# Performance work log

Measured on AMD Instinct MI355X. Metric: run time of the kernel, lower is better.

## Reference

```python
import jax, jax.numpy as jnp
import numpy as np

B, S, D, MD = 4, 4096, 1024, 512
SCALE = 0.02  # init scale for weights


def _layernorm(x, g, b, eps=1e-5):
    m = jnp.mean(x, axis=-1, keepdims=True)
    v = jnp.mean((x - m) ** 2, axis=-1, keepdims=True)
    return (x - m) * jax.lax.rsqrt(v + eps) * g + b


def _mem_mlp(h, W0, W1):
    # MemoryMLP depth=2: linear -> gelu -> linear (no biases)
    return jax.nn.gelu(h @ W0) @ W1


def _assoc_scan(gates, inputs):
    # state_t = g_t * state_{t-1} + in_t, over the seq axis (axis=1)
    def step(state, gi):
        g, i = gi
        s = g * state + i
        return s, s
    init = jnp.zeros_like(inputs[:, 0])
    _, out = jax.lax.scan(step, init, (jnp.moveaxis(gates, 1, 0), jnp.moveaxis(inputs, 1, 0)))
    return jnp.moveaxis(out, 1, 0)


def setup_inputs() -> dict:
    key = jax.random.key(0)
    ks = jax.random.split(key, 10)
    return {
        "x": jax.random.normal(ks[0], (B, S, D), jnp.float32),
        "Wd": jax.random.normal(ks[1], (D, MD), jnp.float32) * SCALE,
        "bd": jnp.zeros((MD,), jnp.float32),
        "Wu": jax.random.normal(ks[2], (MD, D), jnp.float32) * SCALE,
        "bu": jnp.zeros((D,), jnp.float32),
        "Wq": jax.random.normal(ks[3], (MD, MD), jnp.float32) * SCALE,
        "bq": jnp.zeros((MD,), jnp.float32),
        "Wk": jax.random.normal(ks[4], (MD, MD), jnp.float32) * SCALE,
        "bk": jnp.zeros((MD,), jnp.float32),
        "Wv": jax.random.normal(ks[5], (MD, MD), jnp.float32) * SCALE,
        "bv": jnp.zeros((MD,), jnp.float32),
        "q_gamma": jnp.ones((MD,), jnp.float32),
        "q_beta": jnp.zeros((MD,), jnp.float32),
        "k_gamma": jnp.ones((MD,), jnp.float32),
        "k_beta": jnp.zeros((MD,), jnp.float32),
        "W0": jax.random.normal(ks[6], (MD, MD), jnp.float32) * SCALE,
        "W1": jax.random.normal(ks[7], (MD, MD), jnp.float32) * SCALE,
        "adaptive_lr": jnp.full((1,), 0.01, jnp.float32),
        "forget_factor": jnp.full((1,), 0.1, jnp.float32),
    }


def reference(x, Wd, bd, Wu, bu, Wq, bq, Wk, bk, Wv, bv,
              q_gamma, q_beta, k_gamma, k_beta, W0, W1,
              adaptive_lr, forget_factor):
    h = x @ Wd + bd                                   # [B,S,MD] down_proj
    q = _layernorm(h @ Wq + bq, q_gamma, q_beta)      # q_norm(to_queries)
    k = _layernorm(h @ Wk + bk, k_gamma, k_beta)      # k_norm(to_keys)
    v = h @ Wv + bv                                   # to_values
    retrieved = _mem_mlp(q, W0, W1)                   # memory read
    pred = _mem_mlp(k, W0, W1)                        # memory store pred
    # per-token surprise: MSE over feature dim
    surprise = jnp.mean((pred - v) ** 2, axis=-1, keepdims=True)  # [B,S,1]
    gate_val = 1.0 - jax.nn.sigmoid(forget_factor)[0]
    gates = jnp.full((B, S, 1), 1.0, jnp.float32) * gate_val
    inputs = adaptive_lr[0] * surprise * v            # surprise-weighted write
    scanned = _assoc_scan(gates, inputs)              # sequential recurrence
    out = (retrieved + scanned) @ Wu + bu             # up_proj
    return out
```

## Files before the change

kernel.cpp:

```cpp
#include <hip/hip_runtime.h>
#include <hip/hip_bf16.h>
#include <math.h>

#define B_    4
#define S_    4096
#define DD    1024
#define MD    512
#define NTOK  16384
#define CHUNK 32
#define NCH   128

typedef unsigned short u16;
typedef unsigned int u32;
typedef __attribute__((ext_vector_type(8))) short short8;
typedef __attribute__((ext_vector_type(4))) float f32x4;
typedef __attribute__((ext_vector_type(4))) unsigned short us4;

__device__ __forceinline__ float bf2f(u16 u) {
    u32 x = ((u32)u) << 16;
    return __builtin_bit_cast(float, x);
}
__device__ __forceinline__ u16 f2bf(float f) {
    u32 x = __builtin_bit_cast(u32, f);
    u32 lsb = (x >> 16) & 1u;
    x += 0x7fffu + lsb;
    return (u16)(x >> 16);
}
__device__ __forceinline__ float gelu_f(float x) {
    float x3 = x * x * x;
    return 0.5f * x * (1.0f + tanhf(0.7978845608028654f * (x + 0.044715f * x3)));
}
__device__ __forceinline__ float gate_from_ff(const float* ff) {
    return 1.0f - 1.0f / (1.0f + expf(-ff[0]));
}

#define GLDS(gp, lp) __builtin_amdgcn_global_load_lds( \
    (const __attribute__((address_space(1))) void*)(gp), \
    (__attribute__((address_space(3))) void*)(lp), 16, 0, 0)

__device__ __forceinline__ int swzoff(int row, int byteInRow) {
    return ((row * 128 + byteInRow) ^ ((row & 7) << 4)) >> 1;
}

template<int EPI, int HB, int OUTBF>
__global__ __launch_bounds__(256) void gemm_bf16_k(
    const u16* __restrict__ A, const u16* __restrict__ BT,
    const float* __restrict__ bias, void* __restrict__ outp,
    int K, int gx, int OM)
{
    __shared__ __align__(16) u16 Al[2][128 * 64];
    __shared__ __align__(16) u16 Bl[2][128 * 64];
    const int tid = threadIdx.x;
    const int w = tid >> 6, l = tid & 63;

    const int nwg = gridDim.x;
    const int cpx = nwg >> 3;
    const int o = blockIdx.x;
    const int swz = (o & 7) * cpx + (o >> 3);
    const int bx = swz % gx, by = swz / gx;

    const int rowBase = by * 128, colBase = bx * 128;
    const int wm = (w >> 1) * 64, wn = (w & 1) * 64;

    const int srow = l >> 3;
    const int skoff = ((l & 7) ^ (l >> 3)) * 8;
    const u16* Ag[4];
    const u16* Bg[4];
#pragma unroll
    for (int j = 0; j < 4; ++j) {
        const int seg = w * 4 + j;
        Ag[j] = A  + (size_t)(rowBase + seg * 8 + srow) * K + skoff;
        Bg[j] = BT + (size_t)(colBase + seg * 8 + srow) * K + skoff;
    }

    f32x4 acc[4][4];
#pragma unroll
    for (int i = 0; i < 4; ++i)
#pragma unroll
        for (int j = 0; j < 4; ++j) acc[i][j] = (f32x4){0.f, 0.f, 0.f, 0.f};

    const int KT = K >> 6;

#define STAGE(kt, buf) do { \
    const size_t ko = (size_t)(kt) << 6; \
    _Pragma("unroll") \
    for (int j = 0; j < 4; ++j) { \
        GLDS(Ag[j] + ko, &Al[buf][(w * 4 + j) * 512]); \
        GLDS(Bg[j] + ko, &Bl[buf][(w * 4 + j) * 512]); \
    } \
} while (0)

    STAGE(0, 0);
    __syncthreads();

    const int lr = l & 15;
    const int gb = (l >> 4) * 16;
    int cur = 0;
    for (int kt = 0; kt < KT; ++kt) {
        if (kt + 1 < KT) STAGE(kt + 1, cur ^ 1);
#pragma unroll
        for (int ks = 0; ks < 2; ++ks) {
            short8 af[4], bfr[4];
#pragma unroll
            for (int m = 0; m < 4; ++m)
                af[m] = *(const short8*)&Al[cur][swzoff(wm + m * 16 + lr, ks * 64 + gb)];
#pragma unroll
            for (int n = 0; n < 4; ++n)
                bfr[n] = *(const short8*)&Bl[cur][swzoff(wn + n * 16 + lr, ks * 64 + gb)];
#pragma unroll
            for (int m = 0; m < 4; ++m)
#pragma unroll
                for (int n = 0; n < 4; ++n)
                    acc[m][n] = __builtin_amdgcn_mfma_f32_16x16x32_bf16(af[m], bfr[n], acc[m][n], 0, 0, 0);
        }
        __syncthreads();
        cur ^= 1;
    }
#undef STAGE

    const int g4 = (l >> 4) * 4;
    const int col0 = colBase + wn;

    if (OUTBF) {
        u16* scr = &Al[0][0] + w * 1024;
        u16* ob = (u16*)outp;
        const bool odd = l & 1;
        const int lrp = lr & ~1;
#pragma unroll
        for (int m = 0; m < 4; ++m) {
            const int baseRow = rowBase + wm + m * 16;
            float vq[4][4];
#pragma unroll
            for (int n = 0; n < 4; ++n) {
                const float bj = HB ? bias[col0 + n * 16 + lr] : 0.0f;
#pragma unroll
                for (int q = 0; q < 4; ++q) {
                    float vv = acc[m][n][q] + bj;
                    if (EPI == 1) vv = gelu_f(vv);
                    vq[n][q] = vv;
                }
            }
#pragma unroll
            for (int n = 0; n < 4; ++n) {
                float pv[4];
#pragma unroll
                for (int q = 0; q < 4; ++q) pv[q] = __shfl_xor(vq[n][q], 1);
                const int q0 = odd ? 2 : 0;
#pragma unroll
                for (int j = 0; j < 2; ++j) {
                    const int qq = q0 + j;
                    float lo = odd ? pv[qq] : vq[n][qq];
                    float hi = odd ? vq[n][qq] : pv[qq];
                    u32 word = (u32)f2bf(lo) | ((u32)f2bf(hi) << 16);
                    *(u32*)&scr[(g4 + qq) * 64 + n * 16 + lrp] = word;
                }
            }
            asm volatile("s_waitcnt lgkmcnt(0)" ::: "memory");
            __builtin_amdgcn_sched_barrier(0);
            short8 r0 = *(const short8*)&scr[(l >> 3) * 64 + (l & 7) * 8];
            short8 r1 = *(const short8*)&scr[((l >> 3) + 8) * 64 + (l & 7) * 8];
            const size_t gaddr = (size_t)(baseRow + (l >> 3)) * OM + col0 + (l & 7) * 8;
            *(short8*)(ob + gaddr) = r0;
            *(short8*)(ob + gaddr + (size_t)8 * OM) = r1;
            __builtin_amdgcn_sched_barrier(0);
        }
    } else {
#pragma unroll
        for (int n = 0; n < 4; ++n) {
            const int col = col0 + n * 16 + lr;
            const float bj = HB ? bias[col] : 0.0f;
#pragma unroll
            for (int m = 0; m < 4; ++m) {
                const int row0 = rowBase + wm + m * 16 + g4;
#pragma unroll
                for (int q = 0; q < 4; ++q) {
                    float vv = acc[m][n][q] + bj;
                    if (EPI == 1) vv = gelu_f(vv);
                    ((float*)outp)[(size_t)(row0 + q) * OM + col] = vv;
                }
            }
        }
    }
}

__global__ __launch_bounds__(256) void cvt_bf16_k(const float* __restrict__ in,
                                                  u16* __restrict__ out, int n)
{
    size_t i = ((size_t)blockIdx.x * 256 + threadIdx.x) * 8;
    if (i + 8 > (size_t)n) return;
    float4 a = *(const float4*)(in + i);
    float4 b = *(const float4*)(in + i + 4);
    short8 o;
    o[0] = (short)f2bf(a.x); o[1] = (short)f2bf(a.y);
    o[2] = (short)f2bf(a.z); o[3] = (short)f2bf(a.w);
    o[4] = (short)f2bf(b.x); o[5] = (short)f2bf(b.y);
    o[6] = (short)f2bf(b.z); o[7] = (short)f2bf(b.w);
    *(short8*)(out + i) = o;
}

__global__ __launch_bounds__(256) void wtrans_k(const float* __restrict__ W,
                                                u16* __restrict__ WT, int K, int M)
{
    __shared__ float t[32][33];
    const int tx = threadIdx.x, ty = threadIdx.y;
    const int m0 = blockIdx.x * 32, k0 = blockIdx.y * 32;
#pragma unroll
    for (int i = 0; i < 4; ++i)
        t[ty + i * 8][tx] = W[(size_t)(k0 + ty + i * 8) * M + m0 + tx];
    __syncthreads();
#pragma unroll
    for (int i = 0; i < 4; ++i)
        WT[(size_t)(m0 + ty + i * 8) * K + k0 + tx] = f2bf(t[tx][ty + i * 8]);
}

__global__ __launch_bounds__(256) void wtrans5_k(
    const float* __restrict__ Wa, const float* __restrict__ Wb,
    const float* __restrict__ Wc, const float* __restrict__ Wd_,
    const float* __restrict__ We,
    u16* __restrict__ Ta, u16* __restrict__ Tb, u16* __restrict__ Tc,
    u16* __restrict__ Td, u16* __restrict__ Te)
{
    __shared__ float t[32][33];
    const float* W; u16* T;
    switch (blockIdx.z) {
        case 0: W = Wa; T = Ta; break;
        case 1: W = Wb; T = Tb; break;
        case 2: W = Wc; T = Tc; break;
        case 3: W = Wd_; T = Td; break;
        default: W = We; T = Te; break;
    }
    const int tx = threadIdx.x, ty = threadIdx.y;
    const int m0 = blockIdx.x * 32, k0 = blockIdx.y * 32;
#pragma unroll
    for (int i = 0; i < 4; ++i)
        t[ty + i * 8][tx] = W[(size_t)(k0 + ty + i * 8) * 512 + m0 + tx];
    __syncthreads();
#pragma unroll
    for (int i = 0; i < 4; ++i)
        T[(size_t)(m0 + ty + i * 8) * 512 + k0 + tx] = f2bf(t[tx][ty + i * 8]);
}

__global__ __launch_bounds__(256) void ln2_k(u16* __restrict__ X0, u16* __restrict__ X1,
                                             const float* __restrict__ g0, const float* __restrict__ b0,
                                             const float* __restrict__ g1, const float* __restrict__ b1)
{
    const int row = blockIdx.x, tid = threadIdx.x;
    u16* x = (blockIdx.y ? X1 : X0) + (size_t)row * MD;
    const float* g = blockIdx.y ? g1 : g0;
    const float* b = blockIdx.y ? b1 : b0;
    float v0 = bf2f(x[tid]), v1 = bf2f(x[tid + 256]);
    float s = v0 + v1, q = v0 * v0 + v1 * v1;
#pragma unroll
    for (int off = 32; off > 0; off >>= 1) {
        s += __shfl_down(s, off);
        q += __shfl_down(q, off);
    }
    __shared__ float redS[4], redQ[4];
    __shared__ float s_mean, s_rstd;
    const int lane = tid & 63, w = tid >> 6;
    if (lane == 0) { redS[w] = s; redQ[w] = q; }
    __syncthreads();
    if (tid == 0) {
        float S = redS[0] + redS[1] + redS[2] + redS[3];
        float Q = redQ[0] + redQ[1] + redQ[2] + redQ[3];
        float m = S * (1.f / 512.f);
        float var = Q * (1.f / 512.f) - m * m;
        s_mean = m; s_rstd = rsqrtf(var + 1e-5f);
    }
    __syncthreads();
    const float m = s_mean, rs = s_rstd;
    x[tid]       = f2bf((v0 - m) * rs * g[tid]       + b[tid]);
    x[tid + 256] = f2bf((v1 - m) * rs * g[tid + 256] + b[tid + 256]);
}

__global__ __launch_bounds__(256) void surprise_k(const u16* __restrict__ pred,
                                                  const u16* __restrict__ v,
                                                  const float* __restrict__ lr_p,
                                                  float* __restrict__ coef)
{
    const int row = blockIdx.x, tid = threadIdx.x;
    const u16* pp = pred + (size_t)row * MD;
    const u16* vp = v + (size_t)row * MD;
    float d0 = bf2f(pp[tid]) - bf2f(vp[tid]);
    float d1 = bf2f(pp[tid + 256]) - bf2f(vp[tid + 256]);
    float q = d0 * d0 + d1 * d1;
#pragma unroll
    for (int off = 32; off > 0; off >>= 1) q += __shfl_down(q, off);
    __shared__ float redQ[4];
    const int lane = tid & 63, w = tid >> 6;
    if (lane == 0) redQ[w] = q;
    __syncthreads();
    if (tid == 0) {
        float Q = redQ[0] + redQ[1] + redQ[2] + redQ[3];
        coef[row] = lr_p[0] * (Q * (1.f / 512.f));
    }
}

__global__ __launch_bounds__(256) void scan1_k(u16* __restrict__ io,
                                               const float* __restrict__ coef,
                                               const float* __restrict__ ff,
                                               float* __restrict__ carry)
{
    const int idx = blockIdx.x * blockDim.x + threadIdx.x;
    const int d4 = (idx & 127) * 4;
    const int c = (idx >> 7) & (NCH - 1);
    const int b = idx >> 14;
    const float g = gate_from_ff(ff);
    const int tok0 = b * S_ + c * CHUNK;
    u16* p = io + (size_t)tok0 * MD + d4;
    const float* cf = coef + tok0;
    float s0 = 0.f, s1 = 0.f, s2 = 0.f, s3 = 0.f;
#pragma unroll 4
    for (int t = 0; t < CHUNK; ++t) {
        us4 vv = *(const us4*)(p + (size_t)t * MD);
        const float ct = cf[t];
        s0 = fmaf(g, s0, ct * bf2f(vv.x));
        s1 = fmaf(g, s1, ct * bf2f(vv.y));
        s2 = fmaf(g, s2, ct * bf2f(vv.z));
        s3 = fmaf(g, s3, ct * bf2f(vv.w));
        us4 ov = { f2bf(s0), f2bf(s1), f2bf(s2), f2bf(s3) };
        *(us4*)(p + (size_t)t * MD) = ov;
    }
    float4 cw = { s0, s1, s2, s3 };
    *(float4*)(carry + ((size_t)b * NCH + c) * MD + d4) = cw;
}

__global__ __launch_bounds__(256) void scan2_k(const float* __restrict__ carry,
                                               const float* __restrict__ ff,
                                               float* __restrict__ Sin)
{
    const int idx = blockIdx.x * blockDim.x + threadIdx.x;
    const int d = idx & (MD - 1);
    const int b = idx >> 9;
    const float g = gate_from_ff(ff);
    const float gL = powf(g, (float)CHUNK);
    float p = 0.f;
    for (int c = 0; c < NCH; ++c) {
        Sin[((size_t)b * NCH + c) * MD + d] = p;
        p = carry[((size_t)b * NCH + c) * MD + d] + gL * p;
    }
}

__global__ __launch_bounds__(256) void scan3_k(const u16* __restrict__ loc,
                                               const float* __restrict__ Sin,
                                               const u16* __restrict__ retr,
                                               const float* __restrict__ ff,
                                               u16* __restrict__ fin)
{
    const size_t idx = (size_t)blockIdx.x * blockDim.x + threadIdx.x;
    const int d4 = (int)(idx & 127) * 4;
    const int t = (int)((idx >> 7) & (S_ - 1));
    const int b = (int)(idx >> 19);
    const int c = t >> 5, tl = t & (CHUNK - 1);
    const float g = gate_from_ff(ff);
    const float f = exp2f((float)(tl + 1) * log2f(g));
    const size_t row = (size_t)(b * S_ + t) * MD + d4;
    us4 lv = *(const us4*)(loc + row);
    us4 rv = *(const us4*)(retr + row);
    float4 sv = *(const float4*)(Sin + ((size_t)b * NCH + c) * MD + d4);
    us4 ov;
    ov.x = f2bf(bf2f(lv.x) + f * sv.x + bf2f(rv.x));
    ov.y = f2bf(bf2f(lv.y) + f * sv.y + bf2f(rv.y));
    ov.z = f2bf(bf2f(lv.z) + f * sv.z + bf2f(rv.z));
    ov.w = f2bf(bf2f(lv.w) + f * sv.w + bf2f(rv.w));
    *(us4*)(fin + row) = ov;
}

extern "C" void kernel_launch(void* const* d_in, const int* in_sizes, int n_in,
                              void* d_out, int out_size, void* d_ws, size_t ws_size,
                              hipStream_t stream) {
    const float* x   = (const float*)d_in[0];
    const float* Wd  = (const float*)d_in[1];
    const float* bd  = (const float*)d_in[2];
    const float* Wu  = (const float*)d_in[3];
    const float* bu  = (const float*)d_in[4];
    const float* Wq  = (const float*)d_in[5];
    const float* bq  = (const float*)d_in[6];
    const float* Wk  = (const float*)d_in[7];
    const float* bk  = (const float*)d_in[8];
    const float* Wv  = (const float*)d_in[9];
    const float* bv  = (const float*)d_in[10];
    const float* qg  = (const float*)d_in[11];
    const float* qb  = (const float*)d_in[12];
    const float* kg  = (const float*)d_in[13];
    const float* kb  = (const float*)d_in[14];
    const float* W0  = (const float*)d_in[15];
    const float* W1  = (const float*)d_in[16];
    const float* lr  = (const float*)d_in[17];
    const float* ff  = (const float*)d_in[18];
    float* out = (float*)d_out;

    u16* wdT   = (u16*)d_ws;
    u16* wqT   = wdT + 512 * 1024;
    u16* wkT   = wqT + 512 * 512;
    u16* wvT   = wkT + 512 * 512;
    u16* w0T   = wvT + 512 * 512;
    u16* w1T   = w0T + 512 * 512;
    u16* wuT   = w1T + 512 * 512;
    u16* xb    = wuT + 1024 * 512;
    u16* hb    = xb + (size_t)NTOK * DD;
    u16* b1    = hb + (size_t)NTOK * MD;
    u16* b2    = b1 + (size_t)NTOK * MD;
    u16* VB    = b2 + (size_t)NTOK * MD;
    u16* ax    = VB + (size_t)NTOK * MD;
    float* coef  = (float*)(ax + (size_t)NTOK * MD);
    float* carry = coef + NTOK;
    float* Sin   = carry + (size_t)B_ * NCH * MD;

    dim3 blk(256);
    dim3 t32(32, 8);

    cvt_bf16_k<<<(NTOK * DD) / (256 * 8), blk, 0, stream>>>(x, xb, NTOK * DD);
    wtrans_k<<<dim3(16, 32), t32, 0, stream>>>(Wd, wdT, 1024, 512);
    wtrans5_k<<<dim3(16, 16, 5), t32, 0, stream>>>(Wq, Wk, Wv, W0, W1,
        wqT, wkT, wvT, w0T, w1T);
    wtrans_k<<<dim3(32, 16), t32, 0, stream>>>(Wu, wuT, 512, 1024);

    gemm_bf16_k<0, 1, 1><<<dim3(512), blk, 0, stream>>>(xb, wdT, bd, hb, 1024, 4, 512);
    gemm_bf16_k<0, 1, 1><<<dim3(512), blk, 0, stream>>>(hb, wqT, bq, b1, 512, 4, 512);
    gemm_bf16_k<0, 1, 1><<<dim3(512), blk, 0, stream>>>(hb, wkT, bk, b2, 512, 4, 512);
    gemm_bf16_k<0, 1, 1><<<dim3(512), blk, 0, stream>>>(hb, wvT, bv, VB, 512, 4, 512);
    ln2_k<<<dim3(NTOK, 2), blk, 0, stream>>>(b1, b2, qg, qb, kg, kb);
    gemm_bf16_k<1, 0, 1><<<dim3(512), blk, 0, stream>>>(b1, w0T, nullptr, ax, 512, 4, 512);
    gemm_bf16_k<0, 0, 1><<<dim3(512), blk, 0, stream>>>(ax, w1T, nullptr, b1, 512, 4, 512);
    gemm_bf16_k<1, 0, 1><<<dim3(512), blk, 0, stream>>>(b2, w0T, nullptr, ax, 512, 4, 512);
    gemm_bf16_k<0, 0, 1><<<dim3(512), blk, 0, stream>>>(ax, w1T, nullptr, b2, 512, 4, 512);
    surprise_k<<<NTOK, blk, 0, stream>>>(b2, VB, lr, coef);
    scan1_k<<<(B_ * NCH * (MD / 4)) / 256, blk, 0, stream>>>(VB, coef, ff, carry);
    scan2_k<<<(B_ * MD) / 256, blk, 0, stream>>>(carry, ff, Sin);
    scan3_k<<<(NTOK * (MD / 4)) / 256, blk, 0, stream>>>(VB, Sin, b1, ff, ax);
    gemm_bf16_k<0, 1, 0><<<dim3(1024), blk, 0, stream>>>(ax, wuT, bu, out, 512, 8, 1024);
}
```

Measured before the change: 332.8 us.

## Batch independent GEMMs via grid z and use 3-stage BK=32 pipeline

The GEMM kernel now takes three operand sets selected by blockIdx.z, so the Q/K/V projections run as one launch and the two memory-MLP passes are paired per layer. The mainloop switches from a double-buffered K-tile of 64 to a triple-buffered K-tile of 32, with explicit vmcnt waits and a single barrier per step so loads for two tiles ahead overlap compute. Bias is loaded before the loop, and the scratch buffers are reused from xb and hb to make room for two MLP intermediates. This cuts launch count and tail effects and raises occupancy through smaller LDS use, at the cost of more barriers per unit of K work.

```diff
diff --git a/kernel.cpp b/kernel.cpp
--- a/kernel.cpp
+++ b/kernel.cpp
@@ -38,20 +38,24 @@
     (const __attribute__((address_space(1))) void*)(gp), \
     (__attribute__((address_space(3))) void*)(lp), 16, 0, 0)
 
-__device__ __forceinline__ int swzoff(int row, int byteInRow) {
-    return ((row * 128 + byteInRow) ^ ((row & 7) << 4)) >> 1;
-}
-
 template<int EPI, int HB, int OUTBF>
 __global__ __launch_bounds__(256) void gemm_bf16_k(
-    const u16* __restrict__ A, const u16* __restrict__ BT,
-    const float* __restrict__ bias, void* __restrict__ outp,
+    const u16* __restrict__ A0, const u16* __restrict__ A1, const u16* __restrict__ A2,
+    const u16* __restrict__ W0p, const u16* __restrict__ W1p, const u16* __restrict__ W2p,
+    const float* __restrict__ c0, const float* __restrict__ c1, const float* __restrict__ c2,
+    void* __restrict__ o0, void* __restrict__ o1, void* __restrict__ o2,
     int K, int gx, int OM)
 {
-    __shared__ __align__(16) u16 Al[2][128 * 64];
-    __shared__ __align__(16) u16 Bl[2][128 * 64];
+    __shared__ __align__(16) u16 Al[3][128 * 32];
+    __shared__ __align__(16) u16 Bl[3][128 * 32];
     const int tid = threadIdx.x;
     const int w = tid >> 6, l = tid & 63;
+
+    const int z = blockIdx.z;
+    const u16* A      = (z == 0) ? A0 : (z == 1) ? A1 : A2;
+    const u16* BT     = (z == 0) ? W0p : (z == 1) ? W1p : W2p;
+    const float* bias = (z == 0) ? c0 : (z == 1) ? c1 : c2;
+    void* outp        = (z == 0) ? o0 : (z == 1) ? o1 : o2;
 
     const int nwg = gridDim.x;
     const int cpx = nwg >> 3;
@@ -61,17 +65,23 @@
 
     const int rowBase = by * 128, colBase = bx * 128;
     const int wm = (w >> 1) * 64, wn = (w & 1) * 64;
-
-    const int srow = l >> 3;
-    const int skoff = ((l & 7) ^ (l >> 3)) * 8;
-    const u16* Ag[4];
-    const u16* Bg[4];
-#pragma unroll
-    for (int j = 0; j < 4; ++j) {
-        const int seg = w * 4 + j;
-        Ag[j] = A  + (size_t)(rowBase + seg * 8 + srow) * K + skoff;
-        Bg[j] = BT + (size_t)(colBase + seg * 8 + srow) * K + skoff;
-    }
+    const int lr = l & 15;
+
+    float bj[4] = {0.f, 0.f, 0.f, 0.f};
+    if (HB) {
+#pragma unroll
+        for (int n = 0; n < 4; ++n) bj[n] = bias[colBase + wn + n * 16 + lr];
+        asm volatile("" :: "v"(bj[0]), "v"(bj[1]), "v"(bj[2]), "v"(bj[3]));
+    }
+    asm volatile("s_waitcnt vmcnt(0)" ::: "memory");
+    __builtin_amdgcn_sched_barrier(0);
+
+    const int srow = l >> 2;
+    const int skoff = ((l & 3) ^ (srow & 3)) * 8;
+    const u16* Ag0 = A  + (size_t)(rowBase + w * 16 + srow) * K + skoff;
+    const u16* Ag1 = A  + (size_t)(rowBase + (w + 4) * 16 + srow) * K + skoff;
+    const u16* Bg0 = BT + (size_t)(colBase + w * 16 + srow) * K + skoff;
+    const u16* Bg1 = BT + (size_t)(colBase + (w + 4) * 16 + srow) * K + skoff;
 
     f32x4 acc[4][4];
 #pragma unroll
@@ -79,42 +89,47 @@
 #pragma unroll
         for (int j = 0; j < 4; ++j) acc[i][j] = (f32x4){0.f, 0.f, 0.f, 0.f};
 
-    const int KT = K >> 6;
+    const int KT = K >> 5;
 
 #define STAGE(kt, buf) do { \
-    const size_t ko = (size_t)(kt) << 6; \
-    _Pragma("unroll") \
-    for (int j = 0; j < 4; ++j) { \
-        GLDS(Ag[j] + ko, &Al[buf][(w * 4 + j) * 512]); \
-        GLDS(Bg[j] + ko, &Bl[buf][(w * 4 + j) * 512]); \
-    } \
+    const size_t ko = (size_t)(kt) << 5; \
+    GLDS(Ag0 + ko, &Al[buf][(w * 16) * 32]); \
+    GLDS(Ag1 + ko, &Al[buf][((w + 4) * 16) * 32]); \
+    GLDS(Bg0 + ko, &Bl[buf][(w * 16) * 32]); \
+    GLDS(Bg1 + ko, &Bl[buf][((w + 4) * 16) * 32]); \
 } while (0)
 
     STAGE(0, 0);
-    __syncthreads();
-
-    const int lr = l & 15;
-    const int gb = (l >> 4) * 16;
-    int cur = 0;
-    for (int kt = 0; kt < KT; ++kt) {
-        if (kt + 1 < KT) STAGE(kt + 1, cur ^ 1);
-#pragma unroll
-        for (int ks = 0; ks < 2; ++ks) {
-            short8 af[4], bfr[4];
-#pragma unroll
-            for (int m = 0; m < 4; ++m)
-                af[m] = *(const short8*)&Al[cur][swzoff(wm + m * 16 + lr, ks * 64 + gb)];
+    STAGE(1, 1);
+    asm volatile("s_waitcnt vmcnt(4)" ::: "memory");
+    __builtin_amdgcn_sched_barrier(0);
+    __builtin_amdgcn_s_barrier();
+    __builtin_amdgcn_sched_barrier(0);
+
+    const int rsw = (((l >> 4) ^ (l & 3)) << 3);
+    int bt = 0;
+    for (int t = 0; t < KT; ++t) {
+        int bs = bt + 2; if (bs >= 3) bs -= 3;
+        const bool more = (t + 2) < KT;
+        if (more) STAGE(t + 2, bs);
+        short8 af[4], bfr[4];
+#pragma unroll
+        for (int m = 0; m < 4; ++m)
+            af[m] = *(const short8*)&Al[bt][(wm + m * 16 + lr) * 32 + rsw];
+#pragma unroll
+        for (int n = 0; n < 4; ++n)
+            bfr[n] = *(const short8*)&Bl[bt][(wn + n * 16 + lr) * 32 + rsw];
+#pragma unroll
+        for (int m = 0; m < 4; ++m)
 #pragma unroll
             for (int n = 0; n < 4; ++n)
-                bfr[n] = *(const short8*)&Bl[cur][swzoff(wn + n * 16 + lr, ks * 64 + gb)];
-#pragma unroll
-            for (int m = 0; m < 4; ++m)
-#pragma unroll
-                for (int n = 0; n < 4; ++n)
-                    acc[m][n] = __builtin_amdgcn_mfma_f32_16x16x32_bf16(af[m], bfr[n], acc[m][n], 0, 0, 0);
-        }
-        __syncthreads();
-        cur ^= 1;
+                acc[m][n] = __builtin_amdgcn_mfma_f32_16x16x32_bf16(af[m], bfr[n], acc[m][n], 0, 0, 0);
+        if (more) { asm volatile("s_waitcnt vmcnt(4)" ::: "memory"); }
+        else      { asm volatile("s_waitcnt vmcnt(0)" ::: "memory"); }
+        __builtin_amdgcn_sched_barrier(0);
+        __builtin_amdgcn_s_barrier();
+        __builtin_amdgcn_sched_barrier(0);
+        bt = (bt + 1 == 3) ? 0 : bt + 1;
     }
 #undef STAGE
 
@@ -132,10 +147,9 @@
             float vq[4][4];
 #pragma unroll
             for (int n = 0; n < 4; ++n) {
-                const float bj = HB ? bias[col0 + n * 16 + lr] : 0.0f;
 #pragma unroll
                 for (int q = 0; q < 4; ++q) {
-                    float vv = acc[m][n][q] + bj;
+                    float vv = acc[m][n][q] + bj[n];
                     if (EPI == 1) vv = gelu_f(vv);
                     vq[n][q] = vv;
                 }
@@ -168,13 +182,12 @@
 #pragma unroll
         for (int n = 0; n < 4; ++n) {
             const int col = col0 + n * 16 + lr;
-            const float bj = HB ? bias[col] : 0.0f;
 #pragma unroll
             for (int m = 0; m < 4; ++m) {
                 const int row0 = rowBase + wm + m * 16 + g4;
 #pragma unroll
                 for (int q = 0; q < 4; ++q) {
-                    float vv = acc[m][n][q] + bj;
+                    float vv = acc[m][n][q] + bj[n];
                     if (EPI == 1) vv = gelu_f(vv);
                     ((float*)outp)[(size_t)(row0 + q) * OM + col] = vv;
                 }
@@ -402,10 +415,11 @@
     u16* b1    = hb + (size_t)NTOK * MD;
     u16* b2    = b1 + (size_t)NTOK * MD;
     u16* VB    = b2 + (size_t)NTOK * MD;
-    u16* ax    = VB + (size_t)NTOK * MD;
-    float* coef  = (float*)(ax + (size_t)NTOK * MD);
+    float* coef  = (float*)(VB + (size_t)NTOK * MD);
     float* carry = coef + NTOK;
     float* Sin   = carry + (size_t)B_ * NCH * MD;
+    u16* ax0 = xb;
+    u16* ax1 = xb + (size_t)NTOK * MD;
 
     dim3 blk(256);
     dim3 t32(32, 8);
@@ -416,18 +430,19 @@
         wqT, wkT, wvT, w0T, w1T);
     wtrans_k<<<dim3(32, 16), t32, 0, stream>>>(Wu, wuT, 512, 1024);
 
-    gemm_bf16_k<0, 1, 1><<<dim3(512), blk, 0, stream>>>(xb, wdT, bd, hb, 1024, 4, 512);
-    gemm_bf16_k<0, 1, 1><<<dim3(512), blk, 0, stream>>>(hb, wqT, bq, b1, 512, 4, 512);
-    gemm_bf16_k<0, 1, 1><<<dim3(512), blk, 0, stream>>>(hb, wkT, bk, b2, 512, 4, 512);
-    gemm_bf16_k<0, 1, 1><<<dim3(512), blk, 0, stream>>>(hb, wvT, bv, VB, 512, 4, 512);
+    gemm_bf16_k<0, 1, 1><<<dim3(512, 1, 1), blk, 0, stream>>>(
+        xb, xb, xb, wdT, wdT, wdT, bd, bd, bd, hb, hb, hb, 1024, 4, 512);
+    gemm_bf16_k<0, 1, 1><<<dim3(512, 1, 3), blk, 0, stream>>>(
+        hb, hb, hb, wqT, wkT, wvT, bq, bk, bv, b1, b2, VB, 512, 4, 512);
     ln2_k<<<dim3(NTOK, 2), blk, 0, stream>>>(b1, b2, qg, qb, kg, kb);
-    gemm_bf16_k<1, 0, 1><<<dim3(512), blk, 0, stream>>>(b1, w0T, nullptr, ax, 512, 4, 512);
-    gemm_bf16_k<0, 0, 1><<<dim3(512), blk, 0, stream>>>(ax, w1T, nullptr, b1, 512, 4, 512);
-    gemm_bf16_k<1, 0, 1><<<dim3(512), blk, 0, stream>>>(b2, w0T, nullptr, ax, 512, 4, 512);
-    gemm_bf16_k<0, 0, 1><<<dim3(512), blk, 0, stream>>>(ax, w1T, nullptr, b2, 512, 4, 512);
+    gemm_bf16_k<1, 0, 1><<<dim3(512, 1, 2), blk, 0, stream>>>(
+        b1, b2, b2, w0T, w0T, w0T, nullptr, nullptr, nullptr, ax0, ax1, ax1, 512, 4, 512);
+    gemm_bf16_k<0, 0, 1><<<dim3(512, 1, 2), blk, 0, stream>>>(
+        ax0, ax1, ax1, w1T, w1T, w1T, nullptr, nullptr, nullptr, b1, b2, b2, 512, 4, 512);
     surprise_k<<<NTOK, blk, 0, stream>>>(b2, VB, lr, coef);
     scan1_k<<<(B_ * NCH * (MD / 4)) / 256, blk, 0, stream>>>(VB, coef, ff, carry);
     scan2_k<<<(B_ * MD) / 256, blk, 0, stream>>>(carry, ff, Sin);
-    scan3_k<<<(NTOK * (MD / 4)) / 256, blk, 0, stream>>>(VB, Sin, b1, ff, ax);
-    gemm_bf16_k<0, 1, 0><<<dim3(1024), blk, 0, stream>>>(ax, wuT, bu, out, 512, 8, 1024);
-}
+    scan3_k<<<(NTOK * (MD / 4)) / 256, blk, 0, stream>>>(VB, Sin, b1, ff, hb);
+    gemm_bf16_k<0, 1, 0><<<dim3(1024, 1, 1), blk, 0, stream>>>(
+        hb, hb, hb, wuT, wuT, wuT, bu, bu, bu, out, out, out, 512, 8, 1024);
+}
```

Result: no change. 329.6 us (-1.0%).
